# Performance work log

Measured on AMD Instinct MI355X. Metric: run time of the kernel, lower is better.

The kernel has to match this reference:

```python
import jax, jax.numpy as jnp
import numpy as np

N_SRC = 50000
N_DST = 50000
D = 64
E = 800000


def setup_inputs() -> dict:
    key = jax.random.key(0)
    k1, k2, k3, k4, k5 = jax.random.split(key, 5)
    return {
        "h_src": jax.random.normal(k1, (N_SRC, D), dtype=jnp.float32),
        "h_dst": jax.random.normal(k2, (N_DST, D), dtype=jnp.float32),
        "src_idx": jax.random.randint(k3, (E,), 0, N_SRC, dtype=jnp.int64)
        if jax.config.read("jax_enable_x64")
        else jax.random.randint(k3, (E,), 0, N_SRC, dtype=jnp.int32),
        "dst_idx": jax.random.randint(k4, (E,), 0, N_DST, dtype=jnp.int32),
        "W_src": jax.random.normal(k5, (D, D), dtype=jnp.float32) * (2.0 / np.sqrt(2 * D)),  # xavier_normal w/ relu gain
        "b_src": jnp.zeros((D,), dtype=jnp.float32),
    }


def reference(h_src, h_dst, src_idx, dst_idx, W_src, b_src):
    # --- edge attention logits: u_mul_v (elementwise), shape [E, D] ---
    e = h_src[src_idx] * h_dst[dst_idx]
    # --- edge_softmax: softmax over incoming edges of each dst node, per feature dim ---
    emax = jax.ops.segment_max(e, dst_idx, num_segments=N_DST)  # [N_dst, D]
    emax = jnp.where(jnp.isfinite(emax), emax, 0.0)  # empty segments -> -inf; neutralize
    ex = jnp.exp(e - emax[dst_idx])  # [E, D]
    denom = jax.ops.segment_sum(ex, dst_idx, num_segments=N_DST)  # [N_dst, D]
    alpha = ex / denom[dst_idx]  # [E, D]
    # --- transformed src features: relu(W x + b), viewed as [N_src, H=1, D] ---
    feat_src = jax.nn.relu(h_src @ W_src.T + b_src)  # [N_src, D]
    # --- u_mul_e + sum aggregation (H=1 broadcast) ---
    m = feat_src[src_idx] * alpha  # [E, D]
    rst = jax.ops.segment_sum(m, dst_idx, num_segments=N_DST)  # [N_dst, D]
    return rst[:, None, :]  # [N_dst, num_heads=1, out_feats] (dropout in eval mode)
```

## Files before the change

### kernel.cpp

```cpp
#include <hip/hip_runtime.h>
#include <math.h>
#include <stdint.h>

#define D 64
#define WSZ 128
#define WSHIFT 7
#define QCAP 4096
#define EPT 16
#define NWMAX 512

typedef __attribute__((ext_vector_type(8))) short bf16x8;
typedef __attribute__((ext_vector_type(4))) float f32x4;

__device__ inline ushort bf16_rne_u(float v) {
    uint32_t u = __float_as_uint(v);
    return (ushort)((u + 0x7FFFu + ((u >> 16) & 1u)) >> 16);
}

__global__ __launch_bounds__(256) void prep_kernel(const float* __restrict__ h,
                                                   const float* __restrict__ W,
                                                   const float* __restrict__ b,
                                                   const int* __restrict__ src_idx,
                                                   const int* __restrict__ dst_idx,
                                                   uint32_t* __restrict__ packed,
                                                   int* __restrict__ qcnt,
                                                   uint32_t* __restrict__ queue,
                                                   int Nsrc, int Ndst, int E, int packBlocks) {
    __shared__ ushort hT[64 * 64];
    __shared__ ushort wT[64 * 64];
    __shared__ float bs[64];
    __shared__ int wcount[NWMAX];
    __shared__ int wbase[NWMAX];

    if ((int)blockIdx.x < packBlocks) {
        const int t = threadIdx.x;
        const int R0 = blockIdx.x * 64;

        if (t < 64) bs[t] = b[t];
#pragma unroll
        for (int k = 0; k < 4; ++k) {
            int f4 = k * 256 + t;
            int row = f4 >> 4;
            int c4 = (f4 & 15) * 4;
            int grow = min(R0 + row, Nsrc - 1);
            float4 v = reinterpret_cast<const float4*>(h)[(size_t)grow * 16 + (f4 & 15)];
            hT[row * 64 + c4 + 0] = bf16_rne_u(v.x);
            hT[row * 64 + c4 + 1] = bf16_rne_u(v.y);
            hT[row * 64 + c4 + 2] = bf16_rne_u(v.z);
            hT[row * 64 + c4 + 3] = bf16_rne_u(v.w);
            float4 w = reinterpret_cast<const float4*>(W)[f4];
            wT[row * 64 + c4 + 0] = bf16_rne_u(w.x);
            wT[row * 64 + c4 + 1] = bf16_rne_u(w.y);
            wT[row * 64 + c4 + 2] = bf16_rne_u(w.z);
            wT[row * 64 + c4 + 3] = bf16_rne_u(w.w);
        }
        __syncthreads();

        const int wave = t >> 6;
        const int lane = t & 63;
        const int m = lane & 15;
        const int quad = lane >> 4;

        bf16x8 afrag[2];
#pragma unroll
        for (int ks = 0; ks < 2; ++ks)
            afrag[ks] = *reinterpret_cast<const bf16x8*>(&hT[(wave * 16 + m) * 64 + ks * 32 + quad * 8]);

#pragma unroll
        for (int nt = 0; nt < 4; ++nt) {
            const int c0 = nt * 16;
            f32x4 acc = {0.f, 0.f, 0.f, 0.f};
#pragma unroll
            for (int ks = 0; ks < 2; ++ks) {
                bf16x8 bfrag = *reinterpret_cast<const bf16x8*>(&wT[(c0 + m) * 64 + ks * 32 + quad * 8]);
                acc = __builtin_amdgcn_mfma_f32_16x16x32_bf16(afrag[ks], bfrag, acc, 0, 0, 0);
            }
            const int col = c0 + m;
            const float bias = bs[col];
#pragma unroll
            for (int reg = 0; reg < 4; ++reg) {
                const int tr = wave * 16 + quad * 4 + reg;
                const int row = R0 + tr;
                if (row < Nsrc) {
                    float f = fmaxf(acc[reg] + bias, 0.f);
                    uint32_t val = (uint32_t)hT[tr * 64 + col] | ((uint32_t)bf16_rne_u(f) << 16);
                    __builtin_nontemporal_store(val, &packed[(size_t)row * D + col]);
                }
            }
        }
    } else {
        const int bid = (int)blockIdx.x - packBlocks;
        const int t = threadIdx.x;
        for (int k = t; k < NWMAX; k += 256) wcount[k] = 0;
        __syncthreads();

        const int i = bid * 256 + t;
        const int e0 = i * EPT;
        const bool full = (e0 + EPT <= E);

        int4 d0, d1, d2, d3, s0, s1, s2, s3;
        if (full) {
            const int4* dp = reinterpret_cast<const int4*>(dst_idx) + i * 4;
            const int4* sp = reinterpret_cast<const int4*>(src_idx) + i * 4;
            d0 = dp[0]; d1 = dp[1]; d2 = dp[2]; d3 = dp[3];
            s0 = sp[0]; s1 = sp[1]; s2 = sp[2]; s3 = sp[3];
            atomicAdd(&wcount[d0.x >> WSHIFT], 1); atomicAdd(&wcount[d0.y >> WSHIFT], 1);
            atomicAdd(&wcount[d0.z >> WSHIFT], 1); atomicAdd(&wcount[d0.w >> WSHIFT], 1);
            atomicAdd(&wcount[d1.x >> WSHIFT], 1); atomicAdd(&wcount[d1.y >> WSHIFT], 1);
            atomicAdd(&wcount[d1.z >> WSHIFT], 1); atomicAdd(&wcount[d1.w >> WSHIFT], 1);
            atomicAdd(&wcount[d2.x >> WSHIFT], 1); atomicAdd(&wcount[d2.y >> WSHIFT], 1);
            atomicAdd(&wcount[d2.z >> WSHIFT], 1); atomicAdd(&wcount[d2.w >> WSHIFT], 1);
            atomicAdd(&wcount[d3.x >> WSHIFT], 1); atomicAdd(&wcount[d3.y >> WSHIFT], 1);
            atomicAdd(&wcount[d3.z >> WSHIFT], 1); atomicAdd(&wcount[d3.w >> WSHIFT], 1);
        } else {
            for (int e = e0; e < E; ++e) atomicAdd(&wcount[dst_idx[e] >> WSHIFT], 1);
        }
        __syncthreads();

        for (int k = t; k < NWMAX; k += 256) {
            int c = wcount[k];
            wbase[k] = (c > 0) ? atomicAdd(&qcnt[k], c) : 0;
        }
        __syncthreads();

#define EMIT(dv, sv)                                                            \
        {                                                                       \
            int w_ = (dv) >> WSHIFT;                                            \
            int pos_ = atomicAdd(&wbase[w_], 1);                                \
            if (pos_ < QCAP)                                                    \
                queue[(size_t)w_ * QCAP + pos_] =                               \
                    (uint32_t)(sv) | ((uint32_t)((dv) & (WSZ - 1)) << 16);      \
        }
        if (full) {
            EMIT(d0.x, s0.x) EMIT(d0.y, s0.y) EMIT(d0.z, s0.z) EMIT(d0.w, s0.w)
            EMIT(d1.x, s1.x) EMIT(d1.y, s1.y) EMIT(d1.z, s1.z) EMIT(d1.w, s1.w)
            EMIT(d2.x, s2.x) EMIT(d2.y, s2.y) EMIT(d2.z, s2.z) EMIT(d2.w, s2.w)
            EMIT(d3.x, s3.x) EMIT(d3.y, s3.y) EMIT(d3.z, s3.z) EMIT(d3.w, s3.w)
        } else {
            for (int e = e0; e < E; ++e) { EMIT(dst_idx[e], src_idx[e]) }
        }
#undef EMIT
    }
}

__global__ __launch_bounds__(256) void sortwin_kernel(const uint32_t* __restrict__ queue,
                                                      const int* __restrict__ qcnt,
                                                      uint32_t* __restrict__ csr,
                                                      int* __restrict__ cnt,
                                                      int* __restrict__ row_start, int Ndst) {
    __shared__ uint32_t ent[QCAP];
    __shared__ uint32_t srt[QCAP];
    __shared__ int hist[WSZ], sc[WSZ], cur[WSZ];
    const int w = blockIdx.x;
    const int t = threadIdx.x;
    const int n = min(qcnt[w], QCAP);

    for (int k = t; k < n; k += 256) ent[k] = queue[(size_t)w * QCAP + k];
    if (t < WSZ) hist[t] = 0;
    __syncthreads();
    for (int k = t; k < n; k += 256) atomicAdd(&hist[(ent[k] >> 16) & (WSZ - 1)], 1);
    __syncthreads();
    if (t < WSZ) sc[t] = hist[t];
    __syncthreads();
    for (int off = 1; off < WSZ; off <<= 1) {
        int v = (t >= off && t < WSZ) ? sc[t - off] : 0;
        __syncthreads();
        if (t < WSZ) sc[t] += v;
        __syncthreads();
    }
    if (t < WSZ) cur[t] = sc[t] - hist[t];
    __syncthreads();
    for (int k = t; k < n; k += 256) {
        uint32_t e = ent[k];
        int dl = (e >> 16) & (WSZ - 1);
        int pos = atomicAdd(&cur[dl], 1);
        srt[pos] = e & 0xFFFFu;
    }
    __syncthreads();
    const size_t obase = (size_t)w * QCAP;
    for (int k = t; k < n; k += 256) csr[obase + k] = srt[k];
    if (t < WSZ) {
        int j = w * WSZ + t;
        if (j < Ndst) {
            cnt[j] = hist[t];
            row_start[j] = (int)obase + (sc[t] - hist[t]);
        }
    }
}

__device__ inline void stepd(uint32_t u, float y, float& l, float& a) {
    float x = __uint_as_float(u << 16);
    float f = __uint_as_float(u & 0xFFFF0000u);
    float pe = __expf(x * y);
    l += pe;
    a += pe * f;
}

__device__ inline void step4(uint4 u, const float4& y, float4& l, float4& a) {
    stepd(u.x, y.x, l.x, a.x);
    stepd(u.y, y.y, l.y, a.y);
    stepd(u.z, y.z, l.z, a.z);
    stepd(u.w, y.w, l.w, a.w);
}

__global__ __launch_bounds__(256) void gat_main_kernel(const uint32_t* __restrict__ packed,
                                                       const float* __restrict__ h_dst,
                                                       const int* __restrict__ cnt,
                                                       const int* __restrict__ row_start,
                                                       const uint32_t* __restrict__ csr,
                                                       float* __restrict__ out, int Ndst) {
    const int g = threadIdx.x >> 4;
    const int q = threadIdx.x & 15;
    const int j = blockIdx.x * 16 + g;
    if (j >= Ndst) return;

    const float4 y = reinterpret_cast<const float4*>(h_dst + (size_t)j * D)[q];
    const int n = cnt[j];
    const uint32_t* sl = csr + row_start[j];

    float4 l0 = make_float4(0.f, 0.f, 0.f, 0.f), a0 = l0;
    float4 l1 = l0, a1 = l0, l2 = l0, a2 = l0, l3 = l0, a3 = l0;

    int p = 0;
    for (; p + 3 < n; p += 4) {
        uint32_t s0 = sl[p], s1 = sl[p + 1], s2 = sl[p + 2], s3 = sl[p + 3];
        uint4 u0 = reinterpret_cast<const uint4*>(packed + (size_t)s0 * D)[q];
        uint4 u1 = reinterpret_cast<const uint4*>(packed + (size_t)s1 * D)[q];
        uint4 u2 = reinterpret_cast<const uint4*>(packed + (size_t)s2 * D)[q];
        uint4 u3 = reinterpret_cast<const uint4*>(packed + (size_t)s3 * D)[q];
        step4(u0, y, l0, a0);
        step4(u1, y, l1, a1);
        step4(u2, y, l2, a2);
        step4(u3, y, l3, a3);
    }
    for (; p < n; ++p) {
        uint32_t s0 = sl[p];
        uint4 u0 = reinterpret_cast<const uint4*>(packed + (size_t)s0 * D)[q];
        step4(u0, y, l0, a0);
    }

    l0.x += l1.x + l2.x + l3.x; a0.x += a1.x + a2.x + a3.x;
    l0.y += l1.y + l2.y + l3.y; a0.y += a1.y + a2.y + a3.y;
    l0.z += l1.z + l2.z + l3.z; a0.z += a1.z + a2.z + a3.z;
    l0.w += l1.w + l2.w + l3.w; a0.w += a1.w + a2.w + a3.w;

    float4 o;
    o.x = (l0.x > 0.f) ? a0.x / l0.x : 0.f;
    o.y = (l0.y > 0.f) ? a0.y / l0.y : 0.f;
    o.z = (l0.z > 0.f) ? a0.z / l0.z : 0.f;
    o.w = (l0.w > 0.f) ? a0.w / l0.w : 0.f;
    reinterpret_cast<float4*>(out + (size_t)j * D)[q] = o;
}

extern "C" void kernel_launch(void* const* d_in, const int* in_sizes, int n_in,
                              void* d_out, int out_size, void* d_ws, size_t ws_size,
                              hipStream_t stream) {
    const float* h_src = (const float*)d_in[0];
    const float* h_dst = (const float*)d_in[1];
    const int* src_idx = (const int*)d_in[2];
    const int* dst_idx = (const int*)d_in[3];
    const float* W_src = (const float*)d_in[4];
    const float* b_src = (const float*)d_in[5];
    float* out = (float*)d_out;

    const int Nsrc = in_sizes[0] / D;
    const int Ndst = in_sizes[1] / D;
    const int E = in_sizes[2];
    const int NW = (Ndst + WSZ - 1) >> WSHIFT;

    const int packBlocks = (Nsrc + 63) / 64;
    const int binBlocks = (E + 256 * EPT - 1) / (256 * EPT);

    uint32_t* packed   = (uint32_t*)d_ws;
    int*      qcnt     = (int*)(packed + (size_t)Nsrc * D);
    uint32_t* queue    = (uint32_t*)(qcnt + NWMAX);
    uint32_t* csr      = queue + (size_t)NW * QCAP;
    int*      cnt      = (int*)(csr + (size_t)NW * QCAP);
    int*      row_start= cnt + Ndst;

    hipMemsetAsync(qcnt, 0, sizeof(int) * NWMAX, stream);

    prep_kernel<<<packBlocks + binBlocks, 256, 0, stream>>>(
        h_src, W_src, b_src, src_idx, dst_idx, packed, qcnt, queue,
        Nsrc, Ndst, E, packBlocks);
    sortwin_kernel<<<NW, 256, 0, stream>>>(queue, qcnt, csr, cnt, row_start, Ndst);
    gat_main_kernel<<<(Ndst + 15) / 16, 256, 0, stream>>>(packed, h_dst, cnt, row_start,
                                                          csr, out, Ndst);
}
```

Measured before the change: 131.1 us.

## Split packed source features into four column quarters processed by separate blocks

The packed src table is re-laid out as four contiguous quarter-planes of 16 columns each, and the main gather kernel assigns each block one quarter for 64 destination nodes, with 4 threads per node instead of 16. Each quarter-plane (~3.2MB) is meant to fit better in L2/cache, improving reuse of gathered rows across blocks working on the same quarter. In exchange each node's index list and h_dst row are read four times, and each thread now handles one 64-byte segment per edge with less parallelism per node.

```diff
diff --git a/kernel.cpp b/kernel.cpp
--- a/kernel.cpp
+++ b/kernel.cpp
@@ -84,7 +84,8 @@
                 if (row < Nsrc) {
                     float f = fmaxf(acc[reg] + bias, 0.f);
                     uint32_t val = (uint32_t)hT[tr * 64 + col] | ((uint32_t)bf16_rne_u(f) << 16);
-                    __builtin_nontemporal_store(val, &packed[(size_t)row * D + col]);
+                    __builtin_nontemporal_store(val,
+                        &packed[((size_t)nt * Nsrc + row) * 16 + m]);
                 }
             }
         }
@@ -208,15 +209,18 @@
                                                        const int* __restrict__ cnt,
                                                        const int* __restrict__ row_start,
                                                        const uint32_t* __restrict__ csr,
-                                                       float* __restrict__ out, int Ndst) {
-    const int g = threadIdx.x >> 4;
-    const int q = threadIdx.x & 15;
-    const int j = blockIdx.x * 16 + g;
+                                                       float* __restrict__ out,
+                                                       int Nsrc, int Ndst) {
+    const int qtr = blockIdx.x & 3;
+    const int g = threadIdx.x >> 2;
+    const int c = threadIdx.x & 3;
+    const int j = (blockIdx.x >> 2) * 64 + g;
     if (j >= Ndst) return;
 
-    const float4 y = reinterpret_cast<const float4*>(h_dst + (size_t)j * D)[q];
+    const float4 y = reinterpret_cast<const float4*>(h_dst + (size_t)j * D + qtr * 16)[c];
     const int n = cnt[j];
     const uint32_t* sl = csr + row_start[j];
+    const uint32_t* pq = packed + (size_t)qtr * Nsrc * 16;
 
     float4 l0 = make_float4(0.f, 0.f, 0.f, 0.f), a0 = l0;
     float4 l1 = l0, a1 = l0, l2 = l0, a2 = l0, l3 = l0, a3 = l0;
@@ -224,10 +228,10 @@
     int p = 0;
     for (; p + 3 < n; p += 4) {
         uint32_t s0 = sl[p], s1 = sl[p + 1], s2 = sl[p + 2], s3 = sl[p + 3];
-        uint4 u0 = reinterpret_cast<const uint4*>(packed + (size_t)s0 * D)[q];
-        uint4 u1 = reinterpret_cast<const uint4*>(packed + (size_t)s1 * D)[q];
-        uint4 u2 = reinterpret_cast<const uint4*>(packed + (size_t)s2 * D)[q];
-        uint4 u3 = reinterpret_cast<const uint4*>(packed + (size_t)s3 * D)[q];
+        uint4 u0 = reinterpret_cast<const uint4*>(pq + (size_t)s0 * 16)[c];
+        uint4 u1 = reinterpret_cast<const uint4*>(pq + (size_t)s1 * 16)[c];
+        uint4 u2 = reinterpret_cast<const uint4*>(pq + (size_t)s2 * 16)[c];
+        uint4 u3 = reinterpret_cast<const uint4*>(pq + (size_t)s3 * 16)[c];
         step4(u0, y, l0, a0);
         step4(u1, y, l1, a1);
         step4(u2, y, l2, a2);
@@ -235,7 +239,7 @@
     }
     for (; p < n; ++p) {
         uint32_t s0 = sl[p];
-        uint4 u0 = reinterpret_cast<const uint4*>(packed + (size_t)s0 * D)[q];
+        uint4 u0 = reinterpret_cast<const uint4*>(pq + (size_t)s0 * 16)[c];
         step4(u0, y, l0, a0);
     }
 
@@ -249,7 +253,7 @@
     o.y = (l0.y > 0.f) ? a0.y / l0.y : 0.f;
     o.z = (l0.z > 0.f) ? a0.z / l0.z : 0.f;
     o.w = (l0.w > 0.f) ? a0.w / l0.w : 0.f;
-    reinterpret_cast<float4*>(out + (size_t)j * D)[q] = o;
+    reinterpret_cast<float4*>(out + (size_t)j * D + qtr * 16)[c] = o;
 }
 
 extern "C" void kernel_launch(void* const* d_in, const int* in_sizes, int n_in,
@@ -284,6 +288,7 @@
         h_src, W_src, b_src, src_idx, dst_idx, packed, qcnt, queue,
         Nsrc, Ndst, E, packBlocks);
     sortwin_kernel<<<NW, 256, 0, stream>>>(queue, qcnt, csr, cnt, row_start, Ndst);
-    gat_main_kernel<<<(Ndst + 15) / 16, 256, 0, stream>>>(packed, h_dst, cnt, row_start,
-                                                          csr, out, Ndst);
-}
+    const int mainBlocks = ((Ndst + 63) / 64) * 4;
+    gat_main_kernel<<<mainBlocks, 256, 0, stream>>>(packed, h_dst, cnt, row_start,
+                                                    csr, out, Nsrc, Ndst);
+}
```

New measurement: 132.8 us. Within noise of the previous version (+1.3%).

## Fuse per-window sort into aggregation kernel and shrink destination windows

Applied to the files above, without the earlier changes.

Removes the separate sortwin kernel and the global CSR/cnt/row_start arrays. Each block now sorts its window's queue in shared memory and immediately runs the softmax-aggregation for its destinations, reading source indices from LDS. The window size drops to 64 destinations (QCAP 2048, up to 1024 windows) so each block covers four batches of 16 destinations. This saves a kernel launch and a global write/read of the CSR. In exchange there are fewer, longer-running blocks in the main phase, which may lower parallelism and load balance.

```diff
diff --git a/kernel.cpp b/kernel.cpp
--- a/kernel.cpp
+++ b/kernel.cpp
@@ -3,11 +3,11 @@
 #include <stdint.h>
 
 #define D 64
-#define WSZ 128
-#define WSHIFT 7
-#define QCAP 4096
+#define WSZ 64
+#define WSHIFT 6
+#define QCAP 2048
 #define EPT 16
-#define NWMAX 512
+#define NWMAX 1024
 
 typedef __attribute__((ext_vector_type(8))) short bf16x8;
 typedef __attribute__((ext_vector_type(4))) float f32x4;
@@ -25,7 +25,8 @@
                                                    uint32_t* __restrict__ packed,
                                                    int* __restrict__ qcnt,
                                                    uint32_t* __restrict__ queue,
-                                                   int Nsrc, int Ndst, int E, int packBlocks) {
+                                                   int Nsrc, int Ndst, int E,
+                                                   int packBlocks, int NW) {
     __shared__ ushort hT[64 * 64];
     __shared__ ushort wT[64 * 64];
     __shared__ float bs[64];
@@ -91,7 +92,7 @@
     } else {
         const int bid = (int)blockIdx.x - packBlocks;
         const int t = threadIdx.x;
-        for (int k = t; k < NWMAX; k += 256) wcount[k] = 0;
+        for (int k = t; k < NW; k += 256) wcount[k] = 0;
         __syncthreads();
 
         const int i = bid * 256 + t;
@@ -117,7 +118,7 @@
         }
         __syncthreads();
 
-        for (int k = t; k < NWMAX; k += 256) {
+        for (int k = t; k < NW; k += 256) {
             int c = wcount[k];
             wbase[k] = (c > 0) ? atomicAdd(&qcnt[k], c) : 0;
         }
@@ -143,51 +144,6 @@
     }
 }
 
-__global__ __launch_bounds__(256) void sortwin_kernel(const uint32_t* __restrict__ queue,
-                                                      const int* __restrict__ qcnt,
-                                                      uint32_t* __restrict__ csr,
-                                                      int* __restrict__ cnt,
-                                                      int* __restrict__ row_start, int Ndst) {
-    __shared__ uint32_t ent[QCAP];
-    __shared__ uint32_t srt[QCAP];
-    __shared__ int hist[WSZ], sc[WSZ], cur[WSZ];
-    const int w = blockIdx.x;
-    const int t = threadIdx.x;
-    const int n = min(qcnt[w], QCAP);
-
-    for (int k = t; k < n; k += 256) ent[k] = queue[(size_t)w * QCAP + k];
-    if (t < WSZ) hist[t] = 0;
-    __syncthreads();
-    for (int k = t; k < n; k += 256) atomicAdd(&hist[(ent[k] >> 16) & (WSZ - 1)], 1);
-    __syncthreads();
-    if (t < WSZ) sc[t] = hist[t];
-    __syncthreads();
-    for (int off = 1; off < WSZ; off <<= 1) {
-        int v = (t >= off && t < WSZ) ? sc[t - off] : 0;
-        __syncthreads();
-        if (t < WSZ) sc[t] += v;
-        __syncthreads();
-    }
-    if (t < WSZ) cur[t] = sc[t] - hist[t];
-    __syncthreads();
-    for (int k = t; k < n; k += 256) {
-        uint32_t e = ent[k];
-        int dl = (e >> 16) & (WSZ - 1);
-        int pos = atomicAdd(&cur[dl], 1);
-        srt[pos] = e & 0xFFFFu;
-    }
-    __syncthreads();
-    const size_t obase = (size_t)w * QCAP;
-    for (int k = t; k < n; k += 256) csr[obase + k] = srt[k];
-    if (t < WSZ) {
-        int j = w * WSZ + t;
-        if (j < Ndst) {
-            cnt[j] = hist[t];
-            row_start[j] = (int)obase + (sc[t] - hist[t]);
-        }
-    }
-}
-
 __device__ inline void stepd(uint32_t u, float y, float& l, float& a) {
     float x = __uint_as_float(u << 16);
     float f = __uint_as_float(u & 0xFFFF0000u);
@@ -203,53 +159,87 @@
     stepd(u.w, y.w, l.w, a.w);
 }
 
-__global__ __launch_bounds__(256) void gat_main_kernel(const uint32_t* __restrict__ packed,
-                                                       const float* __restrict__ h_dst,
-                                                       const int* __restrict__ cnt,
-                                                       const int* __restrict__ row_start,
-                                                       const uint32_t* __restrict__ csr,
-                                                       float* __restrict__ out, int Ndst) {
-    const int g = threadIdx.x >> 4;
-    const int q = threadIdx.x & 15;
-    const int j = blockIdx.x * 16 + g;
-    if (j >= Ndst) return;
-
-    const float4 y = reinterpret_cast<const float4*>(h_dst + (size_t)j * D)[q];
-    const int n = cnt[j];
-    const uint32_t* sl = csr + row_start[j];
-
-    float4 l0 = make_float4(0.f, 0.f, 0.f, 0.f), a0 = l0;
-    float4 l1 = l0, a1 = l0, l2 = l0, a2 = l0, l3 = l0, a3 = l0;
-
-    int p = 0;
-    for (; p + 3 < n; p += 4) {
-        uint32_t s0 = sl[p], s1 = sl[p + 1], s2 = sl[p + 2], s3 = sl[p + 3];
-        uint4 u0 = reinterpret_cast<const uint4*>(packed + (size_t)s0 * D)[q];
-        uint4 u1 = reinterpret_cast<const uint4*>(packed + (size_t)s1 * D)[q];
-        uint4 u2 = reinterpret_cast<const uint4*>(packed + (size_t)s2 * D)[q];
-        uint4 u3 = reinterpret_cast<const uint4*>(packed + (size_t)s3 * D)[q];
-        step4(u0, y, l0, a0);
-        step4(u1, y, l1, a1);
-        step4(u2, y, l2, a2);
-        step4(u3, y, l3, a3);
-    }
-    for (; p < n; ++p) {
-        uint32_t s0 = sl[p];
-        uint4 u0 = reinterpret_cast<const uint4*>(packed + (size_t)s0 * D)[q];
-        step4(u0, y, l0, a0);
-    }
-
-    l0.x += l1.x + l2.x + l3.x; a0.x += a1.x + a2.x + a3.x;
-    l0.y += l1.y + l2.y + l3.y; a0.y += a1.y + a2.y + a3.y;
-    l0.z += l1.z + l2.z + l3.z; a0.z += a1.z + a2.z + a3.z;
-    l0.w += l1.w + l2.w + l3.w; a0.w += a1.w + a2.w + a3.w;
-
-    float4 o;
-    o.x = (l0.x > 0.f) ? a0.x / l0.x : 0.f;
-    o.y = (l0.y > 0.f) ? a0.y / l0.y : 0.f;
-    o.z = (l0.z > 0.f) ? a0.z / l0.z : 0.f;
-    o.w = (l0.w > 0.f) ? a0.w / l0.w : 0.f;
-    reinterpret_cast<float4*>(out + (size_t)j * D)[q] = o;
+__global__ __launch_bounds__(256) void gat_fused_kernel(const uint32_t* __restrict__ packed,
+                                                        const float* __restrict__ h_dst,
+                                                        const int* __restrict__ qcnt,
+                                                        const uint32_t* __restrict__ queue,
+                                                        float* __restrict__ out, int Ndst) {
+    __shared__ uint32_t ent[QCAP];
+    __shared__ ushort srt[QCAP];
+    __shared__ int hist[WSZ], sc[WSZ], cur[WSZ];
+    const int w = blockIdx.x;
+    const int t = threadIdx.x;
+    const int n = min(qcnt[w], QCAP);
+
+    for (int k = t; k < n; k += 256) ent[k] = queue[(size_t)w * QCAP + k];
+    if (t < WSZ) hist[t] = 0;
+    __syncthreads();
+    for (int k = t; k < n; k += 256) atomicAdd(&hist[(ent[k] >> 16) & (WSZ - 1)], 1);
+    __syncthreads();
+    if (t < WSZ) sc[t] = hist[t];
+    __syncthreads();
+    for (int off = 1; off < WSZ; off <<= 1) {
+        int v = (t >= off && t < WSZ) ? sc[t - off] : 0;
+        __syncthreads();
+        if (t < WSZ) sc[t] += v;
+        __syncthreads();
+    }
+    if (t < WSZ) cur[t] = sc[t] - hist[t];
+    __syncthreads();
+    for (int k = t; k < n; k += 256) {
+        uint32_t e = ent[k];
+        int dl = (e >> 16) & (WSZ - 1);
+        int pos = atomicAdd(&cur[dl], 1);
+        srt[pos] = (ushort)(e & 0xFFFFu);
+    }
+    __syncthreads();
+
+    const int g = t >> 4;
+    const int q = t & 15;
+#pragma unroll
+    for (int bt = 0; bt < 4; ++bt) {
+        const int dl = bt * 16 + g;
+        const int j = w * WSZ + dl;
+        if (j >= Ndst) continue;
+
+        const float4 y = reinterpret_cast<const float4*>(h_dst + (size_t)j * D)[q];
+        const int nd = hist[dl];
+        const int off = sc[dl] - hist[dl];
+
+        float4 l0 = make_float4(0.f, 0.f, 0.f, 0.f), a0 = l0;
+        float4 l1 = l0, a1 = l0, l2 = l0, a2 = l0, l3 = l0, a3 = l0;
+
+        int p = 0;
+        for (; p + 3 < nd; p += 4) {
+            int s0 = srt[off + p], s1 = srt[off + p + 1];
+            int s2 = srt[off + p + 2], s3 = srt[off + p + 3];
+            uint4 u0 = reinterpret_cast<const uint4*>(packed + (size_t)s0 * D)[q];
+            uint4 u1 = reinterpret_cast<const uint4*>(packed + (size_t)s1 * D)[q];
+            uint4 u2 = reinterpret_cast<const uint4*>(packed + (size_t)s2 * D)[q];
+            uint4 u3 = reinterpret_cast<const uint4*>(packed + (size_t)s3 * D)[q];
+            step4(u0, y, l0, a0);
+            step4(u1, y, l1, a1);
+            step4(u2, y, l2, a2);
+            step4(u3, y, l3, a3);
+        }
+        for (; p < nd; ++p) {
+            int s0 = srt[off + p];
+            uint4 u0 = reinterpret_cast<const uint4*>(packed + (size_t)s0 * D)[q];
+            step4(u0, y, l0, a0);
+        }
+
+        l0.x += l1.x + l2.x + l3.x; a0.x += a1.x + a2.x + a3.x;
+        l0.y += l1.y + l2.y + l3.y; a0.y += a1.y + a2.y + a3.y;
+        l0.z += l1.z + l2.z + l3.z; a0.z += a1.z + a2.z + a3.z;
+        l0.w += l1.w + l2.w + l3.w; a0.w += a1.w + a2.w + a3.w;
+
+        float4 o;
+        o.x = (l0.x > 0.f) ? a0.x / l0.x : 0.f;
+        o.y = (l0.y > 0.f) ? a0.y / l0.y : 0.f;
+        o.z = (l0.z > 0.f) ? a0.z / l0.z : 0.f;
+        o.w = (l0.w > 0.f) ? a0.w / l0.w : 0.f;
+        reinterpret_cast<float4*>(out + (size_t)j * D)[q] = o;
+    }
 }
 
 extern "C" void kernel_launch(void* const* d_in, const int* in_sizes, int n_in,
@@ -271,19 +261,14 @@
     const int packBlocks = (Nsrc + 63) / 64;
     const int binBlocks = (E + 256 * EPT - 1) / (256 * EPT);
 
-    uint32_t* packed   = (uint32_t*)d_ws;
-    int*      qcnt     = (int*)(packed + (size_t)Nsrc * D);
-    uint32_t* queue    = (uint32_t*)(qcnt + NWMAX);
-    uint32_t* csr      = queue + (size_t)NW * QCAP;
-    int*      cnt      = (int*)(csr + (size_t)NW * QCAP);
-    int*      row_start= cnt + Ndst;
+    uint32_t* packed = (uint32_t*)d_ws;
+    int*      qcnt   = (int*)(packed + (size_t)Nsrc * D);
+    uint32_t* queue  = (uint32_t*)(qcnt + NWMAX);
 
     hipMemsetAsync(qcnt, 0, sizeof(int) * NWMAX, stream);
 
     prep_kernel<<<packBlocks + binBlocks, 256, 0, stream>>>(
         h_src, W_src, b_src, src_idx, dst_idx, packed, qcnt, queue,
-        Nsrc, Ndst, E, packBlocks);
-    sortwin_kernel<<<NW, 256, 0, stream>>>(queue, qcnt, csr, cnt, row_start, Ndst);
-    gat_main_kernel<<<(Ndst + 15) / 16, 256, 0, stream>>>(packed, h_dst, cnt, row_start,
-                                                          csr, out, Ndst);
-}
+        Nsrc, Ndst, E, packBlocks, NW);
+    gat_fused_kernel<<<NW, 256, 0, stream>>>(packed, h_dst, qcnt, queue, out, Ndst);
+}
```

Result: no change. 131.4 us (+0.2%).
